# Kernel tuning notes

Measured on AMD Instinct MI355X. Metric: run time of the kernel, lower is better.

Reference implementation:

```python
import jax, jax.numpy as jnp
import numpy as np

N_HEADS = 12

def setup_inputs() -> dict:
    key = jax.random.key(0)
    k1, k2, k3 = jax.random.split(key, 3)
    B, S, W = 8, 1024, 768
    x = jax.random.normal(k1, (B, S, W), dtype=jnp.float32)
    w_qkv = jax.random.normal(k2, (W, 3 * W), dtype=jnp.float32) * (W ** -0.5)
    w_out = jax.random.normal(k3, (W, W), dtype=jnp.float32) * (W ** -0.5)
    return {"x": x, "w_qkv": w_qkv, "w_out": w_out}

def reference(x, w_qkv, w_out):
    B, S, W = x.shape
    H = N_HEADS
    D = W // H  # head_width
    scale = W ** -0.5  # NOTE: source scales by width**-0.5, not head_width**-0.5
    qkv = x @ w_qkv  # [B, S, 3W]
    q, k, v = jnp.split(qkv, 3, axis=2)
    q = q.reshape(B, S, H, D)
    k = k.reshape(B, S, H, D)
    # attn_score: [B, i, j, n]
    attn_score = jnp.einsum('binh,bjnh->bijn', q, k) * scale
    attn_weight = jax.nn.softmax(attn_score, axis=2)
    # NOTE: source uses K (not V) here — faithful reproduction of the bug.
    out = jnp.einsum('bijn,bjnh->binh', attn_weight, k)
    out = out.reshape(B, S, W)
    return out @ w_out  # dropout is identity in eval
```

## Files before the change

kernel.cpp:

```cpp
#include <hip/hip_runtime.h>

#define US unsigned short

typedef __bf16 bf16x8 __attribute__((ext_vector_type(8)));
typedef short s16x8 __attribute__((ext_vector_type(8)));
typedef short s16x4 __attribute__((ext_vector_type(4)));
typedef float f32x4 __attribute__((ext_vector_type(4)));

static __device__ __forceinline__ US f2bf(float f) {
  union { float f; unsigned u; } x; x.f = f;
  unsigned r = x.u + 0x7fffu + ((x.u >> 16) & 1u);
  return (US)(r >> 16);
}

static __device__ __forceinline__ unsigned cvtpk(float lo, float hi) {
  unsigned r;
  asm("v_cvt_pk_bf16_f32 %0, %1, %2" : "=v"(r) : "v"(lo), "v"(hi));
  return r;
}

static __device__ __forceinline__ void gload16(const US* g, US* l) {
  __builtin_amdgcn_global_load_lds(
      (const __attribute__((address_space(1))) void*)g,
      (__attribute__((address_space(3))) void*)l, 16, 0, 0);
}

__global__ __launch_bounds__(256) void cast_f32_bf16(
    const float* __restrict__ src, US* __restrict__ dst) {
  int i = blockIdx.x * 256 + threadIdx.x;
  const float4* s = (const float4*)src + (size_t)i * 2;
  float4 a = s[0], b = s[1];
  s16x8 w;
  w[0] = (short)f2bf(a.x); w[1] = (short)f2bf(a.y);
  w[2] = (short)f2bf(a.z); w[3] = (short)f2bf(a.w);
  w[4] = (short)f2bf(b.x); w[5] = (short)f2bf(b.y);
  w[6] = (short)f2bf(b.z); w[7] = (short)f2bf(b.w);
  *(s16x8*)(dst + (size_t)i * 8) = w;
}

__global__ __launch_bounds__(256) void transpose_cast_k(
    const float* __restrict__ src, US* __restrict__ dst, int R, int C,
    float scale, int nlim) {
  __shared__ float t[32][33];
  int n0 = blockIdx.x * 32, r0 = blockIdx.y * 32;
  int tx = threadIdx.x & 31, ty = threadIdx.x >> 5;
  for (int i = 0; i < 4; ++i) {
    int r = i * 8 + ty;
    t[r][tx] = src[(size_t)(r0 + r) * C + n0 + tx];
  }
  __syncthreads();
  for (int i = 0; i < 4; ++i) {
    int n = i * 8 + ty;
    float s = (n0 + n < nlim) ? scale : 1.0f;
    dst[(size_t)(n0 + n) * R + r0 + tx] = f2bf(t[tx][n] * s);
  }
}

__global__ __launch_bounds__(256) void kt_transpose(
    const US* __restrict__ QK, US* __restrict__ KT) {
  __shared__ US t[32][34];
  int bh = blockIdx.z, b = bh / 12, h = bh % 12;
  int s0 = blockIdx.x * 32, d0 = blockIdx.y * 32;
  int tx = threadIdx.x & 31, ty = threadIdx.x >> 5;
  const US* src = QK + ((size_t)b * 1024 + s0) * 1536 + 768 + h * 64 + d0;
  for (int i = 0; i < 4; ++i)
    t[i * 8 + ty][tx] = src[(size_t)(i * 8 + ty) * 1536 + tx];
  __syncthreads();
  US* dst = KT + ((size_t)bh * 64 + d0) * 1024 + s0;
  for (int i = 0; i < 4; ++i)
    dst[(size_t)(i * 8 + ty) * 1024 + tx] = t[tx][i * 8 + ty];
}

template<int OUT_BF16, int FUSE_KT>
__global__ __launch_bounds__(256) void gemm_bt(
    const US* __restrict__ A, const US* __restrict__ Bt,
    void* __restrict__ Cv, int M, int N, int K, US* __restrict__ KT) {
  __shared__ US As[2][128 * 32];
  __shared__ US Bs[2][128 * 32];
  const int tid = threadIdx.x;
  const int wave = tid >> 6, lane = tid & 63;
  const int lr = lane & 15, lg = lane >> 4;
  const int m0 = blockIdx.x * 128, n0 = blockIdx.y * 128;
  const int wr = (wave >> 1) * 64, wc = (wave & 1) * 64;
  const int srow = tid >> 2;
  const int sseg = (tid & 3) ^ (srow & 3);
  const US* gA = A + (size_t)(m0 + srow) * K + sseg * 8;
  const US* gB = Bt + (size_t)(n0 + srow) * K + sseg * 8;

  f32x4 acc[4][4];
  for (int i = 0; i < 4; ++i)
    for (int j = 0; j < 4; ++j) acc[i][j] = (f32x4){0.f, 0.f, 0.f, 0.f};

  const int nIt = K >> 5;
  for (int i = 0; i < 2; ++i) {
    gload16(gA + (size_t)i * 64 * K, &As[0][tid * 8 + i * 2048]);
    gload16(gB + (size_t)i * 64 * K, &Bs[0][tid * 8 + i * 2048]);
  }
  __syncthreads();

  for (int it = 0; it < nIt; ++it) {
    if (it + 1 < nIt) {
      int k0 = (it + 1) * 32, bb = (it + 1) & 1;
      for (int i = 0; i < 2; ++i) {
        gload16(gA + (size_t)i * 64 * K + k0, &As[bb][tid * 8 + i * 2048]);
        gload16(gB + (size_t)i * 64 * K + k0, &Bs[bb][tid * 8 + i * 2048]);
      }
    }
    const US* Ab = As[it & 1];
    const US* Bb = Bs[it & 1];
    bf16x8 af[4], bfr[4];
    for (int mi = 0; mi < 4; ++mi)
      af[mi] = *(const bf16x8*)(Ab + (wr + mi * 16 + lr) * 32 + ((lg ^ (lr & 3)) * 8));
    for (int ni = 0; ni < 4; ++ni)
      bfr[ni] = *(const bf16x8*)(Bb + (wc + ni * 16 + lr) * 32 + ((lg ^ (lr & 3)) * 8));
    for (int mi = 0; mi < 4; ++mi)
      for (int ni = 0; ni < 4; ++ni)
        acc[mi][ni] = __builtin_amdgcn_mfma_f32_16x16x32_bf16(
            af[mi], bfr[ni], acc[mi][ni], 0, 0, 0);
    __syncthreads();
  }

  for (int mi = 0; mi < 4; ++mi)
    for (int ni = 0; ni < 4; ++ni)
      for (int r = 0; r < 4; ++r) {
        size_t row = (size_t)m0 + wr + mi * 16 + lg * 4 + r;
        size_t col = (size_t)n0 + wc + ni * 16 + lr;
        float v = acc[mi][ni][r];
        if (OUT_BF16) ((US*)Cv)[row * N + col] = f2bf(v);
        else          ((float*)Cv)[row * N + col] = v;
      }

  if (FUSE_KT && n0 >= 768) {
    const int h = (n0 + wc - 768) >> 6;
    const int bb = m0 >> 10;
    const int sb = (m0 & 1023) + wr + lg * 4;
    US* ktp = KT + (size_t)(bb * 12 + h) * 64 * 1024;
    for (int mi = 0; mi < 4; ++mi)
      for (int ni = 0; ni < 4; ++ni) {
        int d = ni * 16 + lr;
        s16x4 w;
        w[0] = (short)f2bf(acc[mi][ni][0]);
        w[1] = (short)f2bf(acc[mi][ni][1]);
        w[2] = (short)f2bf(acc[mi][ni][2]);
        w[3] = (short)f2bf(acc[mi][ni][3]);
        *(s16x4*)(ktp + (size_t)d * 1024 + sb + mi * 16) = w;
      }
  }
}

static __device__ __forceinline__ void softmax_route(
    const f32x4 sv[4], float& lsum, bool odd, bool hi, int laneQ0, int laneQ1,
    bf16x8& pa0v, bf16x8& pa1v) {
  float p[4][4];
#pragma unroll
  for (int ns = 0; ns < 4; ++ns)
#pragma unroll
    for (int r = 0; r < 4; ++r) {
      p[ns][r] = __builtin_amdgcn_exp2f(sv[ns][r]);
      lsum += p[ns][r];
    }
  unsigned pk00 = cvtpk(p[0][0], p[0][1]), pk01 = cvtpk(p[0][2], p[0][3]);
  unsigned pk10 = cvtpk(p[1][0], p[1][1]), pk11 = cvtpk(p[1][2], p[1][3]);
  unsigned pk20 = cvtpk(p[2][0], p[2][1]), pk21 = cvtpk(p[2][2], p[2][3]);
  unsigned pk30 = cvtpk(p[3][0], p[3][1]), pk31 = cvtpk(p[3][2], p[3][3]);
  int a0 = (int)(odd ? pk10 : pk00), a1 = (int)(odd ? pk11 : pk01);
  int a2 = (int)(odd ? pk30 : pk20), a3 = (int)(odd ? pk31 : pk21);
  int b0 = (int)(odd ? pk00 : pk10), b1 = (int)(odd ? pk01 : pk11);
  int b2 = (int)(odd ? pk20 : pk30), b3 = (int)(odd ? pk21 : pk31);
  int r0 = __shfl(a0, laneQ0), r1 = __shfl(a1, laneQ0);
  int r2 = __shfl(a2, laneQ0), r3 = __shfl(a3, laneQ0);
  int r4 = __shfl(b0, laneQ1), r5 = __shfl(b1, laneQ1);
  int r6 = __shfl(b2, laneQ1), r7 = __shfl(b3, laneQ1);
  union { unsigned u[4]; bf16x8 v; } pa0, pa1;
  pa0.u[0] = hi ? (unsigned)r4 : (unsigned)r0;
  pa0.u[1] = hi ? (unsigned)r5 : (unsigned)r1;
  pa0.u[2] = hi ? (unsigned)r0 : (unsigned)r4;
  pa0.u[3] = hi ? (unsigned)r1 : (unsigned)r5;
  pa1.u[0] = hi ? (unsigned)r6 : (unsigned)r2;
  pa1.u[1] = hi ? (unsigned)r7 : (unsigned)r3;
  pa1.u[2] = hi ? (unsigned)r2 : (unsigned)r6;
  pa1.u[3] = hi ? (unsigned)r3 : (unsigned)r7;
  pa0v = pa0.v;
  pa1v = pa1.v;
}

__global__ __launch_bounds__(256, 3) void attn_kernel(
    const US* __restrict__ QK, const US* __restrict__ KTg, US* __restrict__ AO) {
  __shared__ US Kr[2][64 * 64];
  __shared__ US Kt[2][64 * 64];
  const int tid = threadIdx.x, wave = tid >> 6, lane = tid & 63;
  const int lr = lane & 15, lg = lane >> 4;
  const int id = blockIdx.y * 8 + blockIdx.x;
  const int bh = (id & 7) * 12 + ((id >> 3) % 12);
  const int qt = id / 96;
  const int b = bh / 12, h = bh % 12;
  const int qw = qt * 128 + wave * 32;
  const size_t rowbase = (size_t)b * 1024;
  const US* Qp = QK + rowbase * 1536 + h * 64;
  const US* Kp = QK + rowbase * 1536 + 768 + h * 64;
  const US* KTp = KTg + (size_t)bh * 64 * 1024;

  const int srow = tid >> 3;
  const int sseg = (tid & 7) ^ (srow & 7);
  const US* gK = Kp + (size_t)srow * 1536 + sseg * 8;
  const US* gT = KTp + (size_t)srow * 1024 + sseg * 8;

  bf16x8 qf0[2], qf1[2];
#pragma unroll
  for (int kk = 0; kk < 2; ++kk) {
    qf0[kk] = *(const bf16x8*)(Qp + (size_t)(qw + lr) * 1536 + kk * 32 + lg * 8);
    qf1[kk] = *(const bf16x8*)(Qp + (size_t)(qw + 16 + lr) * 1536 + kk * 32 + lg * 8);
  }

  const bool odd = (lg & 1) != 0;
  const bool hi = (lg >> 1) != 0;
  const int laneQ0 = lr + 32 * (lg & 1) + 16 * (lg >> 1);
  const int laneQ1 = lr + 32 * (lg & 1) + 16 * (1 - (lg >> 1));

  float lsum0 = 0.f, lsum1 = 0.f;
  f32x4 acc0[4], acc1[4];
#pragma unroll
  for (int d = 0; d < 4; ++d) {
    acc0[d] = (f32x4){0.f, 0.f, 0.f, 0.f};
    acc1[d] = (f32x4){0.f, 0.f, 0.f, 0.f};
  }

  for (int i = 0; i < 2; ++i) {
    gload16(gK + (size_t)(i * 32) * 1536, &Kr[0][tid * 8 + i * 2048]);
    gload16(gT + (size_t)(i * 32) * 1024, &Kt[0][tid * 8 + i * 2048]);
  }
  __syncthreads();

  for (int t = 0; t < 16; ++t) {
    if (t + 1 < 16) {
      int kv0 = (t + 1) * 64, bb = (t + 1) & 1;
      for (int i = 0; i < 2; ++i) {
        gload16(gK + (size_t)(kv0 + i * 32) * 1536, &Kr[bb][tid * 8 + i * 2048]);
        gload16(gT + (size_t)(i * 32) * 1024 + kv0, &Kt[bb][tid * 8 + i * 2048]);
      }
    }
    const US* Krb = Kr[t & 1];
    const US* Ktb = Kt[t & 1];

    f32x4 sv0[4], sv1[4];
    __builtin_amdgcn_s_setprio(1);
#pragma unroll
    for (int ns = 0; ns < 4; ++ns) {
      f32x4 a0 = {0.f, 0.f, 0.f, 0.f}, a1 = {0.f, 0.f, 0.f, 0.f};
#pragma unroll
      for (int kk = 0; kk < 2; ++kk) {
        bf16x8 kf = *(const bf16x8*)(
            Krb + (ns * 16 + lr) * 64 + (((kk * 4 + lg) ^ (lr & 7)) * 8));
        a0 = __builtin_amdgcn_mfma_f32_16x16x32_bf16(kf, qf0[kk], a0, 0, 0, 0);
        a1 = __builtin_amdgcn_mfma_f32_16x16x32_bf16(kf, qf1[kk], a1, 0, 0, 0);
      }
      sv0[ns] = a0; sv1[ns] = a1;
    }
    __builtin_amdgcn_s_setprio(0);

    bf16x8 pa00, pa01, pa10, pa11;
    softmax_route(sv0, lsum0, odd, hi, laneQ0, laneQ1, pa00, pa01);
    softmax_route(sv1, lsum1, odd, hi, laneQ0, laneQ1, pa10, pa11);

    __builtin_amdgcn_s_setprio(1);
#pragma unroll
    for (int d = 0; d < 4; ++d) {
      int drow = d * 16 + lr;
      bf16x8 kf0 = *(const bf16x8*)(Ktb + drow * 64 + ((lg ^ (lr & 7)) * 8));
      bf16x8 kf1 = *(const bf16x8*)(Ktb + drow * 64 + (((4 + lg) ^ (lr & 7)) * 8));
      acc0[d] = __builtin_amdgcn_mfma_f32_16x16x32_bf16(pa00, kf0, acc0[d], 0, 0, 0);
      acc0[d] = __builtin_amdgcn_mfma_f32_16x16x32_bf16(pa01, kf1, acc0[d], 0, 0, 0);
      acc1[d] = __builtin_amdgcn_mfma_f32_16x16x32_bf16(pa10, kf0, acc1[d], 0, 0, 0);
      acc1[d] = __builtin_amdgcn_mfma_f32_16x16x32_bf16(pa11, kf1, acc1[d], 0, 0, 0);
    }
    __builtin_amdgcn_s_setprio(0);
    __syncthreads();
  }

  lsum0 += __shfl_xor(lsum0, 16);
  lsum0 += __shfl_xor(lsum0, 32);
  lsum1 += __shfl_xor(lsum1, 16);
  lsum1 += __shfl_xor(lsum1, 32);
  float inv0[4], inv1[4];
#pragma unroll
  for (int r = 0; r < 4; ++r) {
    inv0[r] = 1.0f / __shfl(lsum0, lg * 4 + r);
    inv1[r] = 1.0f / __shfl(lsum1, lg * 4 + r);
  }
#pragma unroll
  for (int d = 0; d < 4; ++d)
#pragma unroll
    for (int r = 0; r < 4; ++r) {
      size_t row0 = rowbase + qw + lg * 4 + r;
      AO[row0 * 768 + h * 64 + d * 16 + lr] = f2bf(acc0[d][r] * inv0[r]);
      size_t row1 = rowbase + qw + 16 + lg * 4 + r;
      AO[row1 * 768 + h * 64 + d * 16 + lr] = f2bf(acc1[d][r] * inv1[r]);
    }
}

extern "C" void kernel_launch(void* const* d_in, const int* in_sizes, int n_in,
                              void* d_out, int out_size, void* d_ws, size_t ws_size,
                              hipStream_t stream) {
  const float* x    = (const float*)d_in[0];
  const float* wqkv = (const float*)d_in[1];
  const float* wout = (const float*)d_in[2];
  float* out = (float*)d_out;

  US* wqkT  = (US*)d_ws;
  US* woutT = wqkT + (size_t)1536 * 768;
  US* QK    = woutT + (size_t)768 * 768;
  US* AO    = QK + (size_t)8192 * 1536;
  US* xb    = AO + (size_t)8192 * 768;
  const size_t needElems = (size_t)1536 * 768 + (size_t)768 * 768 +
                           (size_t)8192 * 1536 + (size_t)8192 * 768 * 2 +
                           (size_t)96 * 64 * 1024;
  const bool fuse = ws_size >= needElems * sizeof(US);
  US* KT = fuse ? (xb + (size_t)8192 * 768) : xb;

  const float cexp = 0.03608439182435161f * 1.4426950408889634f;

  cast_f32_bf16<<<3072, 256, 0, stream>>>(x, xb);
  transpose_cast_k<<<dim3(48, 24), 256, 0, stream>>>(wqkv, wqkT, 768, 2304, cexp, 768);
  transpose_cast_k<<<dim3(24, 24), 256, 0, stream>>>(wout, woutT, 768, 768, 1.0f, 0);
  if (fuse) {
    gemm_bt<1, 1><<<dim3(64, 12), 256, 0, stream>>>(xb, wqkT, QK, 8192, 1536, 768, KT);
  } else {
    gemm_bt<1, 0><<<dim3(64, 12), 256, 0, stream>>>(xb, wqkT, QK, 8192, 1536, 768, nullptr);
    kt_transpose<<<dim3(32, 2, 96), 256, 0, stream>>>(QK, KT);
  }
  attn_kernel<<<dim3(8, 96), 256, 0, stream>>>(QK, KT, AO);
  gemm_bt<0, 0><<<dim3(64, 6), 256, 0, stream>>>(AO, woutT, out, 8192, 768, 768, nullptr);
}
```

Baseline: 103.2 us.

## Replace QK projection GEMM with 256x256-tile, 512-thread pipelined kernel

Adds a dedicated gemm256 kernel for the QK projection. It uses 256x256 output tiles with 8 waves, a four-slot LDS ring buffer fed by global_load_lds, interleaved prefetch, s_setprio around the MFMA bursts, and explicit waitcnt/barrier scheduling. The goal is more operand reuse per LDS load, fewer blocks, and overlap of global loads with MFMA work. The trade-off is much larger LDS use (128KB) and more accumulator registers, which gives one block per CU and only 192 blocks on 256 CUs, so part of the GPU sits idle. The generic gemm_bt is reduced to the fp32-output path.

```diff
diff --git a/kernel.cpp b/kernel.cpp
--- a/kernel.cpp
+++ b/kernel.cpp
@@ -71,10 +71,139 @@
     dst[(size_t)(i * 8 + ty) * 1024 + tx] = t[tx][i * 8 + ty];
 }
 
-template<int OUT_BF16, int FUSE_KT>
+__global__ __launch_bounds__(512) void gemm256(
+    const US* __restrict__ A, const US* __restrict__ Bt,
+    US* __restrict__ C, US* __restrict__ KT) {
+  const int K = 768, N = 1536;
+  __shared__ US As_[2][2][256 * 32];
+  __shared__ US Bs_[2][2][256 * 32];
+  const int tid = threadIdx.x;
+  const int wave = tid >> 6, lane = tid & 63;
+  const int lr = lane & 15, lg = lane >> 4;
+  const int wm = wave >> 2, wn = wave & 3;
+  const int m0 = blockIdx.x * 256, n0 = blockIdx.y * 256;
+  const US* gA = A + (size_t)m0 * K;
+  const US* gB = Bt + (size_t)n0 * K;
+  const int xsw = (lg ^ (lr & 3)) * 8;
+
+  f32x4 acc[8][4];
+#pragma unroll
+  for (int i = 0; i < 8; ++i)
+#pragma unroll
+    for (int j = 0; j < 4; ++j) acc[i][j] = (f32x4){0.f, 0.f, 0.f, 0.f};
+  bf16x8 afx[4], bfx[4];
+
+  auto STG = [&](US* slot, const US* gbase, int koff) {
+#pragma unroll
+    for (int i = 0; i < 2; ++i) {
+      int s = tid + i * 512;
+      int row = s >> 2;
+      int sg = (s & 3) ^ (row & 3);
+      gload16(gbase + (size_t)row * K + koff + sg * 8, slot + s * 8);
+    }
+  };
+
+#define LDA4(D, KK, MH)                                                      \
+  _Pragma("unroll") for (int mi = 0; mi < 4; ++mi)                           \
+      afx[mi] = *(const bf16x8*)(                                            \
+          &As_[D][KK][(wm * 128 + ((MH)*4 + mi) * 16 + lr) * 32 + xsw]);
+#define LDB4(D, KK)                                                          \
+  _Pragma("unroll") for (int ni = 0; ni < 4; ++ni)                           \
+      bfx[ni] = *(const bf16x8*)(                                            \
+          &Bs_[D][KK][(wn * 64 + ni * 16 + lr) * 32 + xsw]);
+#define MM(MH)                                                               \
+  __builtin_amdgcn_s_barrier();                                              \
+  __builtin_amdgcn_s_setprio(1);                                             \
+  _Pragma("unroll") for (int mi = 0; mi < 4; ++mi)                           \
+      _Pragma("unroll") for (int ni = 0; ni < 4; ++ni)                       \
+          acc[(MH)*4 + mi][ni] = __builtin_amdgcn_mfma_f32_16x16x32_bf16(    \
+              afx[mi], bfx[ni], acc[(MH)*4 + mi][ni], 0, 0, 0);              \
+  __builtin_amdgcn_s_setprio(0);                                             \
+  __builtin_amdgcn_s_barrier();
+
+  STG(Bs_[0][0], gB, 0);
+  STG(As_[0][0], gA, 0);
+  STG(Bs_[0][1], gB, 32);
+  STG(As_[0][1], gA, 32);
+  STG(Bs_[1][0], gB, 64);
+  STG(As_[1][0], gA, 64);
+  STG(Bs_[1][1], gB, 96);
+  asm volatile("s_waitcnt vmcnt(6)" ::: "memory");
+  __builtin_amdgcn_s_barrier();
+
+  for (int it = 0; it < 6; ++it) {
+    const int kb = it * 128;
+    const bool pf = (it < 5);
+    LDB4(0, 0) LDA4(0, 0, 0)
+    STG(As_[1][1], gA, kb + 96);
+    MM(0)
+    LDA4(0, 0, 1)
+    if (pf) STG(Bs_[0][0], gB, kb + 128);
+    MM(1)
+    LDB4(0, 1) LDA4(0, 1, 0)
+    if (pf) STG(As_[0][0], gA, kb + 128);
+    MM(0)
+    LDA4(0, 1, 1)
+    if (pf) {
+      STG(Bs_[0][1], gB, kb + 160);
+      asm volatile("s_waitcnt vmcnt(6)" ::: "memory");
+    } else {
+      asm volatile("s_waitcnt vmcnt(0)" ::: "memory");
+    }
+    MM(1)
+    LDB4(1, 0) LDA4(1, 0, 0)
+    if (pf) STG(As_[0][1], gA, kb + 160);
+    MM(0)
+    LDA4(1, 0, 1)
+    if (pf) STG(Bs_[1][0], gB, kb + 192);
+    MM(1)
+    LDB4(1, 1) LDA4(1, 1, 0)
+    if (pf) STG(As_[1][0], gA, kb + 192);
+    MM(0)
+    LDA4(1, 1, 1)
+    if (pf) {
+      STG(Bs_[1][1], gB, kb + 224);
+      asm volatile("s_waitcnt vmcnt(6)" ::: "memory");
+    }
+    MM(1)
+  }
+
+#pragma unroll
+  for (int mi = 0; mi < 8; ++mi)
+#pragma unroll
+    for (int ni = 0; ni < 4; ++ni)
+#pragma unroll
+      for (int r = 0; r < 4; ++r) {
+        size_t row = (size_t)m0 + wm * 128 + mi * 16 + lg * 4 + r;
+        size_t col = (size_t)n0 + wn * 64 + ni * 16 + lr;
+        C[row * N + col] = f2bf(acc[mi][ni][r]);
+      }
+  if (KT != nullptr && n0 >= 768) {
+    const int h = (n0 + wn * 64 - 768) >> 6;
+    const int bb = m0 >> 10;
+    const int sb = (m0 & 1023) + wm * 128 + lg * 4;
+    US* ktp = KT + (size_t)(bb * 12 + h) * 64 * 1024;
+#pragma unroll
+    for (int mi = 0; mi < 8; ++mi)
+#pragma unroll
+      for (int ni = 0; ni < 4; ++ni) {
+        int d = ni * 16 + lr;
+        s16x4 w;
+        w[0] = (short)f2bf(acc[mi][ni][0]);
+        w[1] = (short)f2bf(acc[mi][ni][1]);
+        w[2] = (short)f2bf(acc[mi][ni][2]);
+        w[3] = (short)f2bf(acc[mi][ni][3]);
+        *(s16x4*)(ktp + (size_t)d * 1024 + sb + mi * 16) = w;
+      }
+  }
+#undef LDA4
+#undef LDB4
+#undef MM
+}
+
 __global__ __launch_bounds__(256) void gemm_bt(
     const US* __restrict__ A, const US* __restrict__ Bt,
-    void* __restrict__ Cv, int M, int N, int K, US* __restrict__ KT) {
+    float* __restrict__ Cv, int M, int N, int K) {
   __shared__ US As[2][128 * 32];
   __shared__ US Bs[2][128 * 32];
   const int tid = threadIdx.x;
@@ -125,27 +254,8 @@
       for (int r = 0; r < 4; ++r) {
         size_t row = (size_t)m0 + wr + mi * 16 + lg * 4 + r;
         size_t col = (size_t)n0 + wc + ni * 16 + lr;
-        float v = acc[mi][ni][r];
-        if (OUT_BF16) ((US*)Cv)[row * N + col] = f2bf(v);
-        else          ((float*)Cv)[row * N + col] = v;
-      }
-
-  if (FUSE_KT && n0 >= 768) {
-    const int h = (n0 + wc - 768) >> 6;
-    const int bb = m0 >> 10;
-    const int sb = (m0 & 1023) + wr + lg * 4;
-    US* ktp = KT + (size_t)(bb * 12 + h) * 64 * 1024;
-    for (int mi = 0; mi < 4; ++mi)
-      for (int ni = 0; ni < 4; ++ni) {
-        int d = ni * 16 + lr;
-        s16x4 w;
-        w[0] = (short)f2bf(acc[mi][ni][0]);
-        w[1] = (short)f2bf(acc[mi][ni][1]);
-        w[2] = (short)f2bf(acc[mi][ni][2]);
-        w[3] = (short)f2bf(acc[mi][ni][3]);
-        *(s16x4*)(ktp + (size_t)d * 1024 + sb + mi * 16) = w;
-      }
-  }
+        Cv[row * N + col] = acc[mi][ni][r];
+      }
 }
 
 static __device__ __forceinline__ void softmax_route(
@@ -323,11 +433,11 @@
   transpose_cast_k<<<dim3(48, 24), 256, 0, stream>>>(wqkv, wqkT, 768, 2304, cexp, 768);
   transpose_cast_k<<<dim3(24, 24), 256, 0, stream>>>(wout, woutT, 768, 768, 1.0f, 0);
   if (fuse) {
-    gemm_bt<1, 1><<<dim3(64, 12), 256, 0, stream>>>(xb, wqkT, QK, 8192, 1536, 768, KT);
+    gemm256<<<dim3(32, 6), 512, 0, stream>>>(xb, wqkT, QK, KT);
   } else {
-    gemm_bt<1, 0><<<dim3(64, 12), 256, 0, stream>>>(xb, wqkT, QK, 8192, 1536, 768, nullptr);
+    gemm256<<<dim3(32, 6), 512, 0, stream>>>(xb, wqkT, QK, nullptr);
     kt_transpose<<<dim3(32, 2, 96), 256, 0, stream>>>(QK, KT);
   }
   attn_kernel<<<dim3(8, 96), 256, 0, stream>>>(QK, KT, AO);
-  gemm_bt<0, 0><<<dim3(64, 6), 256, 0, stream>>>(AO, woutT, out, 8192, 768, 768, nullptr);
-}
+  gemm_bt<<<dim3(64, 6), 256, 0, stream>>>(AO, woutT, out, 8192, 768, 768);
+}
```

Result: slower. 108.3 us (+5.0%).
